# Performance work log

Hardware: AMD Instinct MI355X
Metric: run time of the kernel (lower is better)

Reference implementation:

```python
import jax, jax.numpy as jnp
import numpy as np

N = 16  # lpcoeffs_N, LPC order


def setup_inputs() -> dict:
    key = jax.random.key(0)
    # [B, T, N] LPC coefficients; small magnitude keeps (1 - ki^2) well-conditioned
    x = (jax.random.uniform(key, (64, 32768, N), dtype=jnp.float32) - 0.5) * 0.2
    return {"x": x}


def reference(x):
    # Levinson step-down: LPC -> reflection coefficients (RC).
    # At step i, split into leading j-1 coeffs `a` and already-finalized tail `b`.
    # ki is the current reflection coefficient (first element of the tail).
    for i in range(1, N):
        j = N - i + 1
        a = x[:, :, : j - 1]          # [B, T, j-1]
        b = x[:, :, j - 1 :]          # [B, T, N-j+1]
        ki = b[:, :, 0:1]             # [B, T, 1], broadcasts over last axis
        temp = (a - ki * a[:, :, ::-1]) / (1.0 - ki * ki)
        x = jnp.concatenate([temp, b], axis=2)  # [B, T, N]
    return x
```

## Files before the change

kernel.cpp:

```cpp
#include <hip/hip_runtime.h>


constexpr int N = 16;
constexpr int WAVES_PER_WG = 4;

typedef float f32x4 __attribute__((ext_vector_type(4)));

__device__ __forceinline__ float dpp_xor2(float x) {
    const int xi = __float_as_int(x);
    return __int_as_float(__builtin_amdgcn_update_dpp(xi, xi, 0x4E, 0xF, 0xF, true));
}
__device__ __forceinline__ float dpp_xor1(float x) {
    const int xi = __float_as_int(x);
    return __int_as_float(__builtin_amdgcn_update_dpp(xi, xi, 0xB1, 0xF, 0xF, true));
}

__global__ __launch_bounds__(256, 8) void lpc2rc_kernel(const float* __restrict__ x,
                                                        float* __restrict__ out,
                                                        int nrows) {
    const int tid  = threadIdx.x;
    const int lane = tid & 63;

    const long long wave_row0 = ((long long)blockIdx.x * WAVES_PER_WG + (tid >> 6)) * 64;

    float a[N];

    if (wave_row0 + 64 <= (long long)nrows) {
        const f32x4* __restrict__ in4 = (const f32x4*)x;
        f32x4* __restrict__ out4 = (f32x4*)out;
        const long long base4 = wave_row0 * 4;

        f32x4 ld[4];
#pragma unroll
        for (int c = 0; c < 4; ++c)
            ld[c] = in4[base4 + (long long)(c * 64 + lane)];

        const bool hi = (lane >> 1) & 1;
        const bool lo = lane & 1;

        float W[4][4];
#pragma unroll
        for (int t = 0; t < 4; ++t) {
            const float x0 = dpp_xor2(ld[0][t]);
            const float x1 = dpp_xor2(ld[1][t]);
            const float x2 = dpp_xor2(ld[2][t]);
            const float x3 = dpp_xor2(ld[3][t]);
            W[0][t] = hi ? x2 : ld[0][t];
            W[1][t] = hi ? x3 : ld[1][t];
            W[2][t] = hi ? ld[2][t] : x0;
            W[3][t] = hi ? ld[3][t] : x1;
        }
#pragma unroll
        for (int t = 0; t < 4; ++t) {
            const float y0 = dpp_xor1(W[0][t]);
            const float y1 = dpp_xor1(W[1][t]);
            const float y2 = dpp_xor1(W[2][t]);
            const float y3 = dpp_xor1(W[3][t]);
            a[0  + t] = lo ? y1 : W[0][t];
            a[4  + t] = lo ? W[1][t] : y0;
            a[8  + t] = lo ? y3 : W[2][t];
            a[12 + t] = lo ? W[3][t] : y2;
        }

        float inv_s = 1.0f;
#pragma unroll
        for (int i = 1; i < N; ++i) {
            const int len = N - i;
            const float k = a[len] * inv_s;
            a[len] = k;
            const float r = __builtin_amdgcn_rcpf(1.0f - k * k);
            inv_s *= r;
#pragma unroll
            for (int m = 0; m < len / 2; ++m) {
                const int j = len - 1 - m;
                const float am = a[m];
                const float aj = a[j];
                a[m] = __builtin_fmaf(-k, aj, am);
                a[j] = __builtin_fmaf(-k, am, aj);
            }
            if (len & 1) {
                const int mid = len / 2;
                const float t = a[mid];
                a[mid] = __builtin_fmaf(-k, t, t);
            }
        }
        a[0] *= inv_s;

#pragma unroll
        for (int t = 0; t < 4; ++t) {
            const float x0 = dpp_xor2(a[0  + t]);
            const float x1 = dpp_xor2(a[4  + t]);
            const float x2 = dpp_xor2(a[8  + t]);
            const float x3 = dpp_xor2(a[12 + t]);
            W[0][t] = hi ? x2 : a[0  + t];
            W[1][t] = hi ? x3 : a[4  + t];
            W[2][t] = hi ? a[8  + t] : x0;
            W[3][t] = hi ? a[12 + t] : x1;
        }
        f32x4 st[4];
#pragma unroll
        for (int t = 0; t < 4; ++t) {
            const float y0 = dpp_xor1(W[0][t]);
            const float y1 = dpp_xor1(W[1][t]);
            const float y2 = dpp_xor1(W[2][t]);
            const float y3 = dpp_xor1(W[3][t]);
            st[0][t] = lo ? y1 : W[0][t];
            st[1][t] = lo ? W[1][t] : y0;
            st[2][t] = lo ? y3 : W[2][t];
            st[3][t] = lo ? W[3][t] : y2;
        }

#pragma unroll
        for (int c = 0; c < 4; ++c)
            out4[base4 + (long long)(c * 64 + lane)] = st[c];
    } else {
        const long long r = wave_row0 + lane;
        if (r >= (long long)nrows) return;
        const f32x4* __restrict__ in4 = (const f32x4*)x;
        f32x4* __restrict__ out4 = (f32x4*)out;
        f32x4 v0 = in4[r * 4 + 0], v1 = in4[r * 4 + 1],
              v2 = in4[r * 4 + 2], v3 = in4[r * 4 + 3];
        a[0]=v0.x; a[1]=v0.y; a[2]=v0.z; a[3]=v0.w;
        a[4]=v1.x; a[5]=v1.y; a[6]=v1.z; a[7]=v1.w;
        a[8]=v2.x; a[9]=v2.y; a[10]=v2.z; a[11]=v2.w;
        a[12]=v3.x; a[13]=v3.y; a[14]=v3.z; a[15]=v3.w;

        float inv_s = 1.0f;
#pragma unroll
        for (int i = 1; i < N; ++i) {
            const int len = N - i;
            const float k = a[len] * inv_s;
            a[len] = k;
            const float rr = __builtin_amdgcn_rcpf(1.0f - k * k);
            inv_s *= rr;
#pragma unroll
            for (int m = 0; m < len / 2; ++m) {
                const int j = len - 1 - m;
                const float am = a[m], aj = a[j];
                a[m] = __builtin_fmaf(-k, aj, am);
                a[j] = __builtin_fmaf(-k, am, aj);
            }
            if (len & 1) {
                const int mid = len / 2;
                const float t = a[mid];
                a[mid] = __builtin_fmaf(-k, t, t);
            }
        }
        a[0] *= inv_s;

        v0.x=a[0]; v0.y=a[1]; v0.z=a[2]; v0.w=a[3];
        v1.x=a[4]; v1.y=a[5]; v1.z=a[6]; v1.w=a[7];
        v2.x=a[8]; v2.y=a[9]; v2.z=a[10]; v2.w=a[11];
        v3.x=a[12]; v3.y=a[13]; v3.z=a[14]; v3.w=a[15];
        out4[r * 4 + 0] = v0; out4[r * 4 + 1] = v1;
        out4[r * 4 + 2] = v2; out4[r * 4 + 3] = v3;
    }
}

extern "C" void kernel_launch(void* const* d_in, const int* in_sizes, int n_in,
                              void* d_out, int out_size, void* d_ws, size_t ws_size,
                              hipStream_t stream) {
    const float* x = (const float*)d_in[0];
    float* out = (float*)d_out;
    const int nrows = in_sizes[0] / N;
    const int rows_per_wg = 64 * WAVES_PER_WG;
    const int grid = (nrows + rows_per_wg - 1) / rows_per_wg;
    lpc2rc_kernel<<<grid, 256, 0, stream>>>(x, out, nrows);
}
```

Before: 227.6 us.

## Process four tiles per wave with software-prefetched next-tile loads

Each wave now handles four consecutive 64-row tiles instead of one, so the grid shrinks fourfold. The loads for the next tile are issued before the Levinson recursion on the current tile, overlapping memory latency with compute. The trade-offs are fewer waves in flight and extra registers held for the prefetch buffer, which could reduce occupancy on a memory-bound kernel.

```diff
diff --git a/kernel.cpp b/kernel.cpp
--- a/kernel.cpp
+++ b/kernel.cpp
@@ -3,6 +3,7 @@
 
 constexpr int N = 16;
 constexpr int WAVES_PER_WG = 4;
+constexpr int TILES_PER_WAVE = 4;
 
 typedef float f32x4 __attribute__((ext_vector_type(4)));
 
@@ -15,145 +16,148 @@
     return __int_as_float(__builtin_amdgcn_update_dpp(xi, xi, 0xB1, 0xF, 0xF, true));
 }
 
+__device__ __forceinline__ void levinson16(float a[N]) {
+    float inv_s = 1.0f;
+#pragma unroll
+    for (int i = 1; i < N; ++i) {
+        const int len = N - i;
+        const float k = a[len] * inv_s;
+        a[len] = k;
+        const float r = __builtin_amdgcn_rcpf(1.0f - k * k);
+        inv_s *= r;
+#pragma unroll
+        for (int m = 0; m < len / 2; ++m) {
+            const int j = len - 1 - m;
+            const float am = a[m];
+            const float aj = a[j];
+            a[m] = __builtin_fmaf(-k, aj, am);
+            a[j] = __builtin_fmaf(-k, am, aj);
+        }
+        if (len & 1) {
+            const int mid = len / 2;
+            const float t = a[mid];
+            a[mid] = __builtin_fmaf(-k, t, t);
+        }
+    }
+    a[0] *= inv_s;
+}
+
 __global__ __launch_bounds__(256, 8) void lpc2rc_kernel(const float* __restrict__ x,
                                                         float* __restrict__ out,
                                                         int nrows) {
     const int tid  = threadIdx.x;
     const int lane = tid & 63;
+    const bool hi = (lane >> 1) & 1;
+    const bool lo = lane & 1;
 
-    const long long wave_row0 = ((long long)blockIdx.x * WAVES_PER_WG + (tid >> 6)) * 64;
+    const f32x4* __restrict__ in4 = (const f32x4*)x;
+    f32x4* __restrict__ out4 = (f32x4*)out;
+
+    const long long tile0 =
+        ((long long)blockIdx.x * WAVES_PER_WG + (tid >> 6)) * TILES_PER_WAVE;
 
     float a[N];
+    float W[4][4];
+    f32x4 ld[4];
 
-    if (wave_row0 + 64 <= (long long)nrows) {
-        const f32x4* __restrict__ in4 = (const f32x4*)x;
-        f32x4* __restrict__ out4 = (f32x4*)out;
-        const long long base4 = wave_row0 * 4;
-
-        f32x4 ld[4];
+    {
+        const long long r0 = tile0 * 64;
+        if (r0 + 64 <= (long long)nrows) {
+            const long long b4 = r0 * 4;
 #pragma unroll
-        for (int c = 0; c < 4; ++c)
-            ld[c] = in4[base4 + (long long)(c * 64 + lane)];
-
-        const bool hi = (lane >> 1) & 1;
-        const bool lo = lane & 1;
-
-        float W[4][4];
-#pragma unroll
-        for (int t = 0; t < 4; ++t) {
-            const float x0 = dpp_xor2(ld[0][t]);
-            const float x1 = dpp_xor2(ld[1][t]);
-            const float x2 = dpp_xor2(ld[2][t]);
-            const float x3 = dpp_xor2(ld[3][t]);
-            W[0][t] = hi ? x2 : ld[0][t];
-            W[1][t] = hi ? x3 : ld[1][t];
-            W[2][t] = hi ? ld[2][t] : x0;
-            W[3][t] = hi ? ld[3][t] : x1;
+            for (int c = 0; c < 4; ++c)
+                ld[c] = in4[b4 + (long long)(c * 64 + lane)];
         }
-#pragma unroll
-        for (int t = 0; t < 4; ++t) {
-            const float y0 = dpp_xor1(W[0][t]);
-            const float y1 = dpp_xor1(W[1][t]);
-            const float y2 = dpp_xor1(W[2][t]);
-            const float y3 = dpp_xor1(W[3][t]);
-            a[0  + t] = lo ? y1 : W[0][t];
-            a[4  + t] = lo ? W[1][t] : y0;
-            a[8  + t] = lo ? y3 : W[2][t];
-            a[12 + t] = lo ? W[3][t] : y2;
-        }
-
-        float inv_s = 1.0f;
-#pragma unroll
-        for (int i = 1; i < N; ++i) {
-            const int len = N - i;
-            const float k = a[len] * inv_s;
-            a[len] = k;
-            const float r = __builtin_amdgcn_rcpf(1.0f - k * k);
-            inv_s *= r;
-#pragma unroll
-            for (int m = 0; m < len / 2; ++m) {
-                const int j = len - 1 - m;
-                const float am = a[m];
-                const float aj = a[j];
-                a[m] = __builtin_fmaf(-k, aj, am);
-                a[j] = __builtin_fmaf(-k, am, aj);
-            }
-            if (len & 1) {
-                const int mid = len / 2;
-                const float t = a[mid];
-                a[mid] = __builtin_fmaf(-k, t, t);
-            }
-        }
-        a[0] *= inv_s;
+    }
 
 #pragma unroll
-        for (int t = 0; t < 4; ++t) {
-            const float x0 = dpp_xor2(a[0  + t]);
-            const float x1 = dpp_xor2(a[4  + t]);
-            const float x2 = dpp_xor2(a[8  + t]);
-            const float x3 = dpp_xor2(a[12 + t]);
-            W[0][t] = hi ? x2 : a[0  + t];
-            W[1][t] = hi ? x3 : a[4  + t];
-            W[2][t] = hi ? a[8  + t] : x0;
-            W[3][t] = hi ? a[12 + t] : x1;
-        }
-        f32x4 st[4];
+    for (int t = 0; t < TILES_PER_WAVE; ++t) {
+        const long long r0 = (tile0 + t) * 64;
+        if (r0 >= (long long)nrows) return;
+
+        if (r0 + 64 <= (long long)nrows) {
 #pragma unroll
-        for (int t = 0; t < 4; ++t) {
-            const float y0 = dpp_xor1(W[0][t]);
-            const float y1 = dpp_xor1(W[1][t]);
-            const float y2 = dpp_xor1(W[2][t]);
-            const float y3 = dpp_xor1(W[3][t]);
-            st[0][t] = lo ? y1 : W[0][t];
-            st[1][t] = lo ? W[1][t] : y0;
-            st[2][t] = lo ? y3 : W[2][t];
-            st[3][t] = lo ? W[3][t] : y2;
-        }
+            for (int e = 0; e < 4; ++e) {
+                const float x0 = dpp_xor2(ld[0][e]);
+                const float x1 = dpp_xor2(ld[1][e]);
+                const float x2 = dpp_xor2(ld[2][e]);
+                const float x3 = dpp_xor2(ld[3][e]);
+                W[0][e] = hi ? x2 : ld[0][e];
+                W[1][e] = hi ? x3 : ld[1][e];
+                W[2][e] = hi ? ld[2][e] : x0;
+                W[3][e] = hi ? ld[3][e] : x1;
+            }
+#pragma unroll
+            for (int e = 0; e < 4; ++e) {
+                const float y0 = dpp_xor1(W[0][e]);
+                const float y1 = dpp_xor1(W[1][e]);
+                const float y2 = dpp_xor1(W[2][e]);
+                const float y3 = dpp_xor1(W[3][e]);
+                a[0  + e] = lo ? y1 : W[0][e];
+                a[4  + e] = lo ? W[1][e] : y0;
+                a[8  + e] = lo ? y3 : W[2][e];
+                a[12 + e] = lo ? W[3][e] : y2;
+            }
+
+            if (t + 1 < TILES_PER_WAVE) {
+                const long long r1 = r0 + 64;
+                if (r1 + 64 <= (long long)nrows) {
+                    const long long b4n = r1 * 4;
+#pragma unroll
+                    for (int c = 0; c < 4; ++c)
+                        ld[c] = in4[b4n + (long long)(c * 64 + lane)];
+                }
+            }
+
+            levinson16(a);
 
 #pragma unroll
-        for (int c = 0; c < 4; ++c)
-            out4[base4 + (long long)(c * 64 + lane)] = st[c];
-    } else {
-        const long long r = wave_row0 + lane;
-        if (r >= (long long)nrows) return;
-        const f32x4* __restrict__ in4 = (const f32x4*)x;
-        f32x4* __restrict__ out4 = (f32x4*)out;
-        f32x4 v0 = in4[r * 4 + 0], v1 = in4[r * 4 + 1],
-              v2 = in4[r * 4 + 2], v3 = in4[r * 4 + 3];
-        a[0]=v0.x; a[1]=v0.y; a[2]=v0.z; a[3]=v0.w;
-        a[4]=v1.x; a[5]=v1.y; a[6]=v1.z; a[7]=v1.w;
-        a[8]=v2.x; a[9]=v2.y; a[10]=v2.z; a[11]=v2.w;
-        a[12]=v3.x; a[13]=v3.y; a[14]=v3.z; a[15]=v3.w;
+            for (int e = 0; e < 4; ++e) {
+                const float x0 = dpp_xor2(a[0  + e]);
+                const float x1 = dpp_xor2(a[4  + e]);
+                const float x2 = dpp_xor2(a[8  + e]);
+                const float x3 = dpp_xor2(a[12 + e]);
+                W[0][e] = hi ? x2 : a[0  + e];
+                W[1][e] = hi ? x3 : a[4  + e];
+                W[2][e] = hi ? a[8  + e] : x0;
+                W[3][e] = hi ? a[12 + e] : x1;
+            }
+            f32x4 st[4];
+#pragma unroll
+            for (int e = 0; e < 4; ++e) {
+                const float y0 = dpp_xor1(W[0][e]);
+                const float y1 = dpp_xor1(W[1][e]);
+                const float y2 = dpp_xor1(W[2][e]);
+                const float y3 = dpp_xor1(W[3][e]);
+                st[0][e] = lo ? y1 : W[0][e];
+                st[1][e] = lo ? W[1][e] : y0;
+                st[2][e] = lo ? y3 : W[2][e];
+                st[3][e] = lo ? W[3][e] : y2;
+            }
 
-        float inv_s = 1.0f;
+            const long long b4 = r0 * 4;
 #pragma unroll
-        for (int i = 1; i < N; ++i) {
-            const int len = N - i;
-            const float k = a[len] * inv_s;
-            a[len] = k;
-            const float rr = __builtin_amdgcn_rcpf(1.0f - k * k);
-            inv_s *= rr;
-#pragma unroll
-            for (int m = 0; m < len / 2; ++m) {
-                const int j = len - 1 - m;
-                const float am = a[m], aj = a[j];
-                a[m] = __builtin_fmaf(-k, aj, am);
-                a[j] = __builtin_fmaf(-k, am, aj);
+            for (int c = 0; c < 4; ++c)
+                out4[b4 + (long long)(c * 64 + lane)] = st[c];
+        } else {
+            const long long r = r0 + lane;
+            if (r < (long long)nrows) {
+                f32x4 v0 = in4[r * 4 + 0], v1 = in4[r * 4 + 1],
+                      v2 = in4[r * 4 + 2], v3 = in4[r * 4 + 3];
+                a[0]=v0.x; a[1]=v0.y; a[2]=v0.z; a[3]=v0.w;
+                a[4]=v1.x; a[5]=v1.y; a[6]=v1.z; a[7]=v1.w;
+                a[8]=v2.x; a[9]=v2.y; a[10]=v2.z; a[11]=v2.w;
+                a[12]=v3.x; a[13]=v3.y; a[14]=v3.z; a[15]=v3.w;
+                levinson16(a);
+                v0.x=a[0]; v0.y=a[1]; v0.z=a[2]; v0.w=a[3];
+                v1.x=a[4]; v1.y=a[5]; v1.z=a[6]; v1.w=a[7];
+                v2.x=a[8]; v2.y=a[9]; v2.z=a[10]; v2.w=a[11];
+                v3.x=a[12]; v3.y=a[13]; v3.z=a[14]; v3.w=a[15];
+                out4[r * 4 + 0] = v0; out4[r * 4 + 1] = v1;
+                out4[r * 4 + 2] = v2; out4[r * 4 + 3] = v3;
             }
-            if (len & 1) {
-                const int mid = len / 2;
-                const float t = a[mid];
-                a[mid] = __builtin_fmaf(-k, t, t);
-            }
+            return;
         }
-        a[0] *= inv_s;
-
-        v0.x=a[0]; v0.y=a[1]; v0.z=a[2]; v0.w=a[3];
-        v1.x=a[4]; v1.y=a[5]; v1.z=a[6]; v1.w=a[7];
-        v2.x=a[8]; v2.y=a[9]; v2.z=a[10]; v2.w=a[11];
-        v3.x=a[12]; v3.y=a[13]; v3.z=a[14]; v3.w=a[15];
-        out4[r * 4 + 0] = v0; out4[r * 4 + 1] = v1;
-        out4[r * 4 + 2] = v2; out4[r * 4 + 3] = v3;
     }
 }
 
@@ -163,7 +167,7 @@
     const float* x = (const float*)d_in[0];
     float* out = (float*)d_out;
     const int nrows = in_sizes[0] / N;
-    const int rows_per_wg = 64 * WAVES_PER_WG;
+    const int rows_per_wg = 64 * WAVES_PER_WG * TILES_PER_WAVE;
     const int grid = (nrows + rows_per_wg - 1) / rows_per_wg;
     lpc2rc_kernel<<<grid, 256, 0, stream>>>(x, out, nrows);
 }
```

Result: no change. 230.9 us (+1.5%).
